# Performance work log

Measured on AMD Instinct MI355X. Metric: run time of the kernel, lower is better.

Reference implementation:

```python
import math
import jax, jax.numpy as jnp
import numpy as np

B, S, G, D = 16, 256, 2048, 512
H = 8
DK = D // H  # per-head key dim
E = 8        # num experts
TOPK = 2


def setup_inputs() -> dict:
    key = jax.random.key(0)
    ks = jax.random.split(key, 12)
    init = lambda k, shape, fan_in: jax.random.uniform(k, shape, jnp.float32, -1.0, 1.0) / np.sqrt(fan_in)
    return {
        'query': jax.random.normal(ks[0], (B, S, D), jnp.float32),
        'key': jax.random.normal(ks[1], (B, G, D), jnp.float32),
        'value': jax.random.normal(ks[2], (B, G, D), jnp.float32),  # unused by module (MHA uses h=key)
        'logit_key': jax.random.normal(ks[3], (B, G, D), jnp.float32),
        'attn_mask': jnp.zeros((B, G), dtype=bool),
        'Wq': init(ks[4], (H, D, DK), D),
        'Wk': init(ks[5], (H, D, DK), D),
        'Wv': init(ks[6], (H, D, DK), D),
        'Wo': init(ks[7], (H, DK, D), DK),
        'w_gate': jnp.zeros((D, E), jnp.float32) + init(ks[8], (D, E), D) * 0.0 + init(ks[9], (D, E), D),
        'expert_w': init(ks[10], (E, D, D), D),
    }


def _mha_glimpse(query, h, attn_mask, Wq, Wk, Wv, Wo):
    # Kool-style MHA: K and V both derived from h
    Q = jnp.einsum('bsd,hdk->bhsk', query, Wq)
    K = jnp.einsum('bgd,hdk->bhgk', h, Wk)
    V = jnp.einsum('bgd,hdk->bhgk', h, Wv)
    scores = jnp.einsum('bhsk,bhgk->bhsg', Q, K) / math.sqrt(DK)
    # 2D mask (B,G) expanded over heads and steps; True = masked out
    mask = attn_mask[:, None, None, :]
    scores = jnp.where(mask, jnp.float32(-1e9), scores)
    attn = jax.nn.softmax(scores, axis=-1)
    heads = jnp.einsum('bhsg,bhgk->bhsk', attn, V)
    return jnp.einsum('bhsk,hkd->bsd', heads, Wo)


def _moe(x, w_gate, expert_w):
    # x: (N, D). Noisy top-k gating, eval mode (no noise): clean logits -> top-k -> softmax over top-k.
    logits = x @ w_gate                                  # (N, E)
    top_vals, top_idx = jax.lax.top_k(logits, TOPK)      # (N, k)
    top_gates = jax.nn.softmax(top_vals, axis=-1)        # (N, k)
    gates = jnp.sum(jax.nn.one_hot(top_idx, E, dtype=x.dtype) * top_gates[..., None], axis=1)  # (N, E)
    expert_out = jnp.einsum('nd,edo->neo', x, expert_w)  # dense combine: same math as dispatch/scatter
    return jnp.einsum('ne,neo->no', gates, expert_out)


def reference(query, key, value, logit_key, attn_mask, Wq, Wk, Wv, Wo, w_gate, expert_w):
    glimpse = _mha_glimpse(query, key, attn_mask, Wq, Wk, Wv, Wo)  # (B, S, D)
    gm = _moe(glimpse.reshape(B * S, D), w_gate, expert_w).reshape(B, S, D)
    logits = jnp.einsum('bsd,bgd->bsg', gm, logit_key) / math.sqrt(D)
    return logits
```

## Files before the change

kernel.cpp:

```cpp
#include <hip/hip_runtime.h>

#define B_  16
#define S_  256
#define G_  2048
#define D_  512
#define H_  8
#define DK_ 64
#define E_  8

typedef _Float16 half8  __attribute__((ext_vector_type(8)));
typedef _Float16 half4v __attribute__((ext_vector_type(4)));
typedef float    floatx4 __attribute__((ext_vector_type(4)));
typedef float    floatx16 __attribute__((ext_vector_type(16)));

#define GLDS(g, l) __builtin_amdgcn_global_load_lds( \
    (const __attribute__((address_space(1))) void*)(g), \
    (__attribute__((address_space(3))) void*)(l), 16, 0, 0)

__global__ void __launch_bounds__(256) split_f16(
    const float* __restrict__ src, _Float16* __restrict__ hi,
    _Float16* __restrict__ lo, int n4)
{
    int i = blockIdx.x * 256 + threadIdx.x;
    if (i >= n4) return;
    float4 v = ((const float4*)src)[i];
    half4v h, l;
    h[0] = (_Float16)v.x; h[1] = (_Float16)v.y;
    h[2] = (_Float16)v.z; h[3] = (_Float16)v.w;
    l[0] = (_Float16)(v.x - (float)h[0]); l[1] = (_Float16)(v.y - (float)h[1]);
    l[2] = (_Float16)(v.z - (float)h[2]); l[3] = (_Float16)(v.w - (float)h[3]);
    ((half4v*)hi)[i] = h;
    ((half4v*)lo)[i] = l;
}

__global__ void __launch_bounds__(256) transpose_split(
    const float* __restrict__ src, _Float16* __restrict__ hi,
    _Float16* __restrict__ lo, int R, int C)
{
    __shared__ float T[32][33];
    const int tid = threadIdx.x;
    const long zo = (long)blockIdx.z * R * C;
    const int r0 = blockIdx.y * 32, c0 = blockIdx.x * 32;
#pragma unroll
    for (int p = 0; p < 4; ++p) {
        int i = tid + p * 256;
        int lr = i >> 5, lc = i & 31;
        T[lr][lc] = src[zo + (long)(r0 + lr) * C + (c0 + lc)];
    }
    __syncthreads();
#pragma unroll
    for (int p = 0; p < 4; ++p) {
        int i = tid + p * 256;
        int orr = i >> 5, oc = i & 31;
        float v = T[oc][orr];
        _Float16 h = (_Float16)v;
        long o = zo + (long)(c0 + orr) * R + (r0 + oc);
        hi[o] = h;
        lo[o] = (_Float16)(v - (float)h);
    }
}

__global__ void __launch_bounds__(512) mask_bitmap(
    const unsigned char* __restrict__ mask, unsigned long long* __restrict__ bmp)
{
    const int t = threadIdx.x;
    const int b = t >> 5, tile = t & 31;
    const unsigned char* m = mask + (long)b * G_ + tile * 64;
    unsigned long long v = 0ULL;
#pragma unroll
    for (int i = 0; i < 64; ++i)
        v |= (unsigned long long)(m[i] ? 1u : 0u) << i;
    bmp[t] = v;
}

__global__ void __launch_bounds__(256) gemm_f16x3(
    const _Float16* __restrict__ Ah, const _Float16* __restrict__ Al,
    const _Float16* __restrict__ Bh, const _Float16* __restrict__ Bl,
    float* __restrict__ C, _Float16* __restrict__ Chi, _Float16* __restrict__ Clo,
    long ldc, long sAz, long sBz, long sCz, float alpha)
{
    __shared__ _Float16 Ash[128 * 32], Asl[128 * 32];
    __shared__ _Float16 Bsh[128 * 32], Bsl[128 * 32];
    const int tid = threadIdx.x;
    const int w = tid >> 6, lane = tid & 63;
    const int quad = lane >> 4, tn = lane & 15;
    const int wm = (w >> 1) * 64, wn = (w & 1) * 64;
    const int z = blockIdx.z;
    const long m0 = (long)blockIdx.y * 128;
    const long n0 = (long)blockIdx.x * 128;
    const _Float16* Agh = Ah + (z * sAz + m0) * 512;
    const _Float16* Agl = Al + (z * sAz + m0) * 512;
    const _Float16* Bgh = Bh + (z * sBz + n0) * 512;
    const _Float16* Bgl = Bl + (z * sBz + n0) * 512;
    const long glane = (long)(lane >> 2) * 512 + (lane & 3) * 8;

    floatx4 acc[4][4] = {};

    for (int k0 = 0; k0 < 512; k0 += 32) {
#pragma unroll
        for (int cc = 0; cc < 2; ++cc) {
            const int c = 2 * w + cc;
            const long go = (long)c * 16 * 512 + glane + k0;
            GLDS(Agh + go, Ash + c * 512);
            GLDS(Agl + go, Asl + c * 512);
            GLDS(Bgh + go, Bsh + c * 512);
            GLDS(Bgl + go, Bsl + c * 512);
        }
        asm volatile("s_waitcnt vmcnt(0)" ::: "memory");
        __syncthreads();

        half8 ah[4], al[4], bh[4], bl[4];
#pragma unroll
        for (int t = 0; t < 4; ++t) {
            ah[t] = *(const half8*)&Ash[(wm + t * 16 + tn) * 32 + quad * 8];
            al[t] = *(const half8*)&Asl[(wm + t * 16 + tn) * 32 + quad * 8];
            bh[t] = *(const half8*)&Bsh[(wn + t * 16 + tn) * 32 + quad * 8];
            bl[t] = *(const half8*)&Bsl[(wn + t * 16 + tn) * 32 + quad * 8];
        }
#pragma unroll
        for (int i = 0; i < 4; ++i)
#pragma unroll
            for (int j = 0; j < 4; ++j) {
                acc[i][j] = __builtin_amdgcn_mfma_f32_16x16x32_f16(ah[i], bh[j], acc[i][j], 0, 0, 0);
                acc[i][j] = __builtin_amdgcn_mfma_f32_16x16x32_f16(ah[i], bl[j], acc[i][j], 0, 0, 0);
                acc[i][j] = __builtin_amdgcn_mfma_f32_16x16x32_f16(al[i], bh[j], acc[i][j], 0, 0, 0);
            }
        __syncthreads();
    }

#pragma unroll
    for (int i = 0; i < 4; ++i) {
        const long row0 = m0 + wm + i * 16 + quad * 4;
#pragma unroll
        for (int r = 0; r < 4; ++r) {
            const long row = row0 + r;
#pragma unroll
            for (int j = 0; j < 4; ++j) {
                float v = acc[i][j][r] * alpha;
                const long o = (long)z * sCz + row * ldc + n0 + wn + j * 16 + tn;
                if (C) C[o] = v;
                if (Chi) {
                    _Float16 hh = (_Float16)v;
                    Chi[o] = hh;
                    Clo[o] = (_Float16)(v - (float)hh);
                }
            }
        }
    }
}

__global__ void __launch_bounds__(256) flash_mfma(
    const _Float16* __restrict__ qh, const _Float16* __restrict__ qlo,
    const _Float16* __restrict__ kh, const _Float16* __restrict__ kl,
    const _Float16* __restrict__ vh, const _Float16* __restrict__ vl,
    const unsigned long long* __restrict__ bmp,
    float* __restrict__ Opart, float* __restrict__ Lpart)
{
    __shared__ half8 KH[512], KL[512], VH[512], VL[512];
    const int tid = threadIdx.x;
    const int wid = tid >> 6, lane = tid & 63;
    const int lh = lane >> 5, ln = lane & 31;
    const int head = blockIdx.y, b = blockIdx.z;
    const int sblk = blockIdx.x & 1, gq = blockIdx.x >> 1;
    const long tok0 = (long)b * S_ + sblk * 128 + wid * 32;

    const long qoff = (tok0 + ln) * 512 + head * 64 + lh * 8;
    half8 qfh[4], qfl[4];
#pragma unroll
    for (int ks = 0; ks < 4; ++ks) {
        qfh[ks] = *(const half8*)(qh + qoff + ks * 16);
        qfl[ks] = *(const half8*)(qlo + qoff + ks * 16);
    }

    const int srow_lo = lane >> 3;
    const int sgs = lane & 7;
    const long kgK = (long)b * G_ * 512 + head * 64;
    const long kgV = (long)head * 64 * (B_ * G_) + (long)b * G_;

    floatx16 accO[2] = {};
    float lsum = 0.f;

    for (int t = 0; t < 8; ++t) {
        const int g0 = gq * 512 + t * 64;
#pragma unroll
        for (int cc = 0; cc < 2; ++cc) {
            const int c = 2 * wid + cc;
            const int r = c * 8 + srow_lo;
            const int gs = sgs ^ (r & 7);
            const long ko = kgK + (long)(g0 + r) * 512 + gs * 8;
            const long vo = kgV + (long)r * (B_ * G_) + g0 + gs * 8;
            GLDS(kh + ko, KH + c * 64);
            GLDS(kl + ko, KL + c * 64);
            GLDS(vh + vo, VH + c * 64);
            GLDS(vl + vo, VL + c * 64);
        }
        asm volatile("s_waitcnt vmcnt(0)" ::: "memory");
        __syncthreads();

        floatx16 accS[2] = {};
#pragma unroll
        for (int gt = 0; gt < 2; ++gt) {
            const int grow = gt * 32 + ln;
            const int gbase = grow * 8, gswz = grow & 7;
#pragma unroll
            for (int ks = 0; ks < 4; ++ks) {
                const int gi = gbase + ((ks * 2 + lh) ^ gswz);
                half8 kbh = KH[gi], kbl = KL[gi];
                accS[gt] = __builtin_amdgcn_mfma_f32_32x32x16_f16(kbh, qfh[ks], accS[gt], 0, 0, 0);
                accS[gt] = __builtin_amdgcn_mfma_f32_32x32x16_f16(kbh, qfl[ks], accS[gt], 0, 0, 0);
                accS[gt] = __builtin_amdgcn_mfma_f32_32x32x16_f16(kbl, qfh[ks], accS[gt], 0, 0, 0);
            }
        }

        const unsigned long long bm = bmp[(b << 5) + (g0 >> 6)];
        if (bm != 0ULL) {
            const unsigned w0 = lh ? ((unsigned)bm >> 4) : (unsigned)bm;
            const unsigned w1 = lh ? ((unsigned)(bm >> 32) >> 4) : (unsigned)(bm >> 32);
#pragma unroll
            for (int gt = 0; gt < 2; ++gt) {
                const unsigned wsel = gt ? w1 : w0;
#pragma unroll
                for (int r = 0; r < 16; ++r) {
                    const int sh = (r & 3) + 8 * (r >> 2);
                    if ((wsel >> sh) & 1u) accS[gt][r] = -1.0e9f;
                }
            }
        }

        float rs = 0.f;
#pragma unroll
        for (int gt = 0; gt < 2; ++gt)
#pragma unroll
            for (int r = 0; r < 16; ++r) {
                const float pv = __builtin_exp2f(accS[gt][r]);
                accS[gt][r] = pv;
                rs += pv;
            }
        rs += __shfl_xor(rs, 32);
        lsum += rs;

#pragma unroll
        for (int gt = 0; gt < 2; ++gt)
#pragma unroll
            for (int w = 0; w < 2; ++w) {
                half8 ph, pl;
#pragma unroll
                for (int j = 0; j < 4; ++j) {
                    const float pA = accS[gt][8 * w + j];
                    const float pB = accS[gt][8 * w + 4 + j];
                    const float snd = lh ? pA : pB;
                    const float rcv = __shfl_xor(snd, 32);
                    const float e03 = lh ? rcv : pA;
                    const float e47 = lh ? pB : rcv;
                    float hi = __uint_as_float(__float_as_uint(e03) & 0xFFFFE000u);
                    ph[j] = (_Float16)hi;
                    pl[j] = (_Float16)(e03 - hi);
                    hi = __uint_as_float(__float_as_uint(e47) & 0xFFFFE000u);
                    ph[4 + j] = (_Float16)hi;
                    pl[4 + j] = (_Float16)(e47 - hi);
                }
                const int gvb = gt * 4 + w * 2 + lh;
#pragma unroll
                for (int nt = 0; nt < 2; ++nt) {
                    const int vrow = nt * 32 + ln;
                    const int gi = vrow * 8 + (gvb ^ (vrow & 7));
                    half8 vbh = VH[gi], vbl = VL[gi];
                    accO[nt] = __builtin_amdgcn_mfma_f32_32x32x16_f16(ph, vbh, accO[nt], 0, 0, 0);
                    accO[nt] = __builtin_amdgcn_mfma_f32_32x32x16_f16(ph, vbl, accO[nt], 0, 0, 0);
                    accO[nt] = __builtin_amdgcn_mfma_f32_32x32x16_f16(pl, vbh, accO[nt], 0, 0, 0);
                }
            }
        __syncthreads();
    }

    float* Op = Opart + (long)gq * (4096L * 512);
#pragma unroll
    for (int nt = 0; nt < 2; ++nt)
#pragma unroll
        for (int r = 0; r < 16; ++r) {
            const int s = (r & 3) + 8 * (r >> 2) + 4 * lh;
            Op[(tok0 + s) * 512 + head * 64 + nt * 32 + ln] = accO[nt][r];
        }
    if (lane < 32)
        Lpart[(long)gq * 32768 + (tok0 + lane) * 8 + head] = lsum;
}

__global__ void __launch_bounds__(256) combine_flash(
    const float* __restrict__ Op, const float* __restrict__ Lp,
    _Float16* __restrict__ hd_hi, _Float16* __restrict__ hd_lo)
{
    const int idx = blockIdx.x * 256 + threadIdx.x;
    const int n = idx >> 7;
    const int c = (idx & 127) * 4;
    const int h = c >> 6;
    float l = 0.f;
#pragma unroll
    for (int q = 0; q < 4; ++q) l += Lp[q * 32768 + (long)n * 8 + h];
    const float inv = 1.0f / l;
    float4 a = *(const float4*)(Op + (long)n * 512 + c);
#pragma unroll
    for (int q = 1; q < 4; ++q) {
        float4 d = *(const float4*)(Op + (long)q * 2097152 + (long)n * 512 + c);
        a.x += d.x; a.y += d.y; a.z += d.z; a.w += d.w;
    }
    const float ox = a.x * inv, oy = a.y * inv, oz = a.z * inv, ow = a.w * inv;
    half4v hh, ll;
    hh[0] = (_Float16)ox; hh[1] = (_Float16)oy;
    hh[2] = (_Float16)oz; hh[3] = (_Float16)ow;
    ll[0] = (_Float16)(ox - (float)hh[0]); ll[1] = (_Float16)(oy - (float)hh[1]);
    ll[2] = (_Float16)(oz - (float)hh[2]); ll[3] = (_Float16)(ow - (float)hh[3]);
    *(half4v*)(hd_hi + (long)n * 512 + c) = hh;
    *(half4v*)(hd_lo + (long)n * 512 + c) = ll;
}

__global__ void __launch_bounds__(256) gate_topk(
    const _Float16* __restrict__ Xh, const _Float16* __restrict__ Xl,
    const float* __restrict__ wg, float* __restrict__ gates)
{
    __shared__ float W[512][8];
    __shared__ float Xs[256][37];
    const int tid = threadIdx.x;
    const int n0 = blockIdx.x * 256;
#pragma unroll
    for (int p = 0; p < 16; ++p) ((float*)W)[tid + p * 256] = wg[tid + p * 256];

    float acc[8] = {};
    for (int dc = 0; dc < 512; dc += 32) {
        __syncthreads();
#pragma unroll
        for (int p = 0; p < 8; ++p) {
            int f = tid + p * 256;
            int row = f >> 3, c4 = f & 7;
            long o = (long)(n0 + row) * 512 + dc + 4 * c4;
            half4v hv = *(const half4v*)(Xh + o);
            half4v lv = *(const half4v*)(Xl + o);
#pragma unroll
            for (int i = 0; i < 4; ++i) Xs[row][4 * c4 + i] = (float)hv[i] + (float)lv[i];
        }
        __syncthreads();
        for (int d2 = 0; d2 < 32; ++d2) {
            float xv = Xs[tid][d2];
#pragma unroll
            for (int e = 0; e < 8; ++e) acc[e] += xv * W[dc + d2][e];
        }
    }
    float v1 = -3.0e38f; int i1 = 0;
#pragma unroll
    for (int e = 0; e < 8; ++e) if (acc[e] > v1) { v1 = acc[e]; i1 = e; }
    float v2 = -3.0e38f; int i2 = -1;
#pragma unroll
    for (int e = 0; e < 8; ++e) if (e != i1 && acc[e] > v2) { v2 = acc[e]; i2 = e; }
    float t = __expf(v2 - v1);
    float g1 = 1.0f / (1.0f + t);
    float g2 = t / (1.0f + t);
#pragma unroll
    for (int e = 0; e < 8; ++e)
        gates[(long)(n0 + tid) * 8 + e] = (e == i1) ? g1 : ((e == i2) ? g2 : 0.0f);
}

__global__ void __launch_bounds__(256) combine_moe(
    const float* __restrict__ eo, const float* __restrict__ gates,
    _Float16* __restrict__ gh, _Float16* __restrict__ gl)
{
    const int idx = blockIdx.x * 256 + threadIdx.x;
    const int n = idx >> 7;
    const int c = (idx & 127) * 4;
    float g[8];
#pragma unroll
    for (int e = 0; e < 8; ++e) g[e] = gates[(long)n * 8 + e];
    float ax = 0.f, ay = 0.f, az = 0.f, aw = 0.f;
#pragma unroll
    for (int e = 0; e < 8; ++e) {
        if (g[e] != 0.0f) {
            float4 v = *(const float4*)(eo + (long)e * 2097152 + (long)n * 512 + c);
            ax += g[e] * v.x; ay += g[e] * v.y; az += g[e] * v.z; aw += g[e] * v.w;
        }
    }
    half4v h, l;
    h[0] = (_Float16)ax; h[1] = (_Float16)ay; h[2] = (_Float16)az; h[3] = (_Float16)aw;
    l[0] = (_Float16)(ax - (float)h[0]); l[1] = (_Float16)(ay - (float)h[1]);
    l[2] = (_Float16)(az - (float)h[2]); l[3] = (_Float16)(aw - (float)h[3]);
    *(half4v*)(gh + (long)n * 512 + c) = h;
    *(half4v*)(gl + (long)n * 512 + c) = l;
}

extern "C" void kernel_launch(void* const* d_in, const int* in_sizes, int n_in,
                              void* d_out, int out_size, void* d_ws, size_t ws_size,
                              hipStream_t stream) {
    const float* query     = (const float*)d_in[0];
    const float* key       = (const float*)d_in[1];
    const float* logit_key = (const float*)d_in[3];
    const unsigned char* mask = (const unsigned char*)d_in[4];
    const float* Wq = (const float*)d_in[5];
    const float* Wk = (const float*)d_in[6];
    const float* Wv = (const float*)d_in[7];
    const float* Wo = (const float*)d_in[8];
    const float* wg = (const float*)d_in[9];
    const float* Ew = (const float*)d_in[10];
    float* out = (float*)d_out;

    const size_t MBy = 1048576;
    char* W = (char*)d_ws;
    _Float16* q_hi  = (_Float16*)(W + 0 * MBy);
    _Float16* q_lo  = (_Float16*)(W + 4 * MBy);
    _Float16* kp_hi = (_Float16*)(W + 8 * MBy);
    _Float16* kp_lo = (_Float16*)(W + 40 * MBy);
    _Float16* vt_hi = (_Float16*)(W + 72 * MBy);
    _Float16* vt_lo = (_Float16*)(W + 104 * MBy);
    _Float16* kin_hi = (_Float16*)(W + 136 * MBy);
    _Float16* kin_lo = (_Float16*)(W + 168 * MBy);
    float*    Opart = (float*)(W + 136 * MBy);
    float*    Lpart = (float*)(W + 168 * MBy);
    float*    eo    = (float*)(W + 136 * MBy);
    _Float16* lk_hi = (_Float16*)(W + 136 * MBy);
    _Float16* lk_lo = (_Float16*)(W + 168 * MBy);
    _Float16* wq_hi = (_Float16*)(W + 204 * MBy);
    _Float16* wq_lo = (_Float16*)(W + 204 * MBy + 524288);
    _Float16* wk_hi = (_Float16*)(W + 205 * MBy);
    _Float16* wk_lo = (_Float16*)(W + 205 * MBy + 524288);
    _Float16* wv_hi = (_Float16*)(W + 206 * MBy);
    _Float16* wv_lo = (_Float16*)(W + 206 * MBy + 524288);
    _Float16* wo_hi = (_Float16*)(W + 207 * MBy);
    _Float16* wo_lo = (_Float16*)(W + 207 * MBy + 524288);
    _Float16* ew_hi = (_Float16*)(W + 208 * MBy);
    _Float16* ew_lo = (_Float16*)(W + 212 * MBy);
    _Float16* qi_hi = (_Float16*)(W + 216 * MBy);
    _Float16* qi_lo = (_Float16*)(W + 220 * MBy);
    _Float16* hd_hi = (_Float16*)(W + 216 * MBy);
    _Float16* hd_lo = (_Float16*)(W + 220 * MBy);
    _Float16* gl_hi = (_Float16*)(W + 224 * MBy);
    _Float16* gl_lo = (_Float16*)(W + 228 * MBy);
    _Float16* gm_hi = (_Float16*)(W + 232 * MBy);
    _Float16* gm_lo = (_Float16*)(W + 236 * MBy);
    float*    gates = (float*)(W + 240 * MBy);
    unsigned long long* bmp = (unsigned long long*)(W + 240 * MBy + 131072);

    dim3 blk(256);

    split_f16<<<dim3(16384), blk, 0, stream>>>(key, kin_hi, kin_lo, 4194304);
    split_f16<<<dim3(2048), blk, 0, stream>>>(query, qi_hi, qi_lo, 524288);
    mask_bitmap<<<dim3(1), dim3(512), 0, stream>>>(mask, bmp);
    transpose_split<<<dim3(2, 16, 8), blk, 0, stream>>>(Wq, wq_hi, wq_lo, 512, 64);
    transpose_split<<<dim3(2, 16, 8), blk, 0, stream>>>(Wk, wk_hi, wk_lo, 512, 64);
    transpose_split<<<dim3(2, 16, 8), blk, 0, stream>>>(Wv, wv_hi, wv_lo, 512, 64);
    transpose_split<<<dim3(16, 16, 1), blk, 0, stream>>>(Wo, wo_hi, wo_lo, 512, 512);
    transpose_split<<<dim3(16, 16, 8), blk, 0, stream>>>(Ew, ew_hi, ew_lo, 512, 512);

    gemm_f16x3<<<dim3(4, 32, 1), blk, 0, stream>>>(
        qi_hi, qi_lo, wq_hi, wq_lo, nullptr, q_hi, q_lo, 512, 0, 0, 0,
        0.1803368801111204f);
    gemm_f16x3<<<dim3(4, 256, 1), blk, 0, stream>>>(
        kin_hi, kin_lo, wk_hi, wk_lo, nullptr, kp_hi, kp_lo, 512, 0, 0, 0, 1.0f);
    gemm_f16x3<<<dim3(256, 4, 1), blk, 0, stream>>>(
        wv_hi, wv_lo, kin_hi, kin_lo, nullptr, vt_hi, vt_lo, (long)B_ * G_,
        0, 0, 0, 1.0f);

    flash_mfma<<<dim3(8, H_, B_), blk, 0, stream>>>(
        q_hi, q_lo, kp_hi, kp_lo, vt_hi, vt_lo, bmp, Opart, Lpart);
    combine_flash<<<dim3(2048), blk, 0, stream>>>(Opart, Lpart, hd_hi, hd_lo);

    gemm_f16x3<<<dim3(4, 32, 1), blk, 0, stream>>>(
        hd_hi, hd_lo, wo_hi, wo_lo, nullptr, gl_hi, gl_lo, 512, 0, 0, 0, 1.0f);

    gate_topk<<<dim3(16), blk, 0, stream>>>(gl_hi, gl_lo, wg, gates);

    gemm_f16x3<<<dim3(4, 32, 8), blk, 0, stream>>>(
        gl_hi, gl_lo, ew_hi, ew_lo, eo, nullptr, nullptr, 512, 0, 512, 2097152, 1.0f);

    combine_moe<<<dim3(2048), blk, 0, stream>>>(eo, gates, gm_hi, gm_lo);

    split_f16<<<dim3(16384), blk, 0, stream>>>(logit_key, lk_hi, lk_lo, 4194304);

    gemm_f16x3<<<dim3(16, 2, 16), blk, 0, stream>>>(
        gm_hi, gm_lo, lk_hi, lk_lo, out, nullptr, nullptr, 2048,
        256, 2048, 524288, 0.04419417382415922f);
}
```

Measured before the change: 617.6 us.

## Replace dense MoE expert GEMM with sparse top-2 token dispatch

Gating now emits top-2 expert indices and gates, and a new kernel builds per-expert token lists with atomics. A gathered GEMM then computes only the routed tokens for each expert, skipping empty tiles, and the combine step reads just the two relevant expert outputs. This removes roughly three quarters of the expert GEMM FLOPs and eo traffic. The cost is an extra launch, atomics, gathered row loads, and load imbalance across experts.

```diff
diff --git a/kernel.cpp b/kernel.cpp
--- a/kernel.cpp
+++ b/kernel.cpp
@@ -61,9 +61,11 @@
 }
 
 __global__ void __launch_bounds__(512) mask_bitmap(
-    const unsigned char* __restrict__ mask, unsigned long long* __restrict__ bmp)
+    const unsigned char* __restrict__ mask, unsigned long long* __restrict__ bmp,
+    int* __restrict__ cnt)
 {
     const int t = threadIdx.x;
+    if (t < 8) cnt[t] = 0;
     const int b = t >> 5, tile = t & 31;
     const unsigned char* m = mask + (long)b * G_ + tile * 64;
     unsigned long long v = 0ULL;
@@ -145,6 +147,83 @@
                     Clo[o] = (_Float16)(v - (float)hh);
                 }
             }
+        }
+    }
+}
+
+__global__ void __launch_bounds__(256) gemm_moe(
+    const _Float16* __restrict__ Ah, const _Float16* __restrict__ Al,
+    const _Float16* __restrict__ Bh, const _Float16* __restrict__ Bl,
+    float* __restrict__ eo, const int* __restrict__ lists,
+    const int* __restrict__ cnt)
+{
+    const int e = blockIdx.z;
+    const int n_e = cnt[e];
+    const int tile = blockIdx.y;
+    if (tile * 128 >= n_e) return;
+
+    __shared__ _Float16 Ash[128 * 32], Asl[128 * 32];
+    __shared__ _Float16 Bsh[128 * 32], Bsl[128 * 32];
+    const int tid = threadIdx.x;
+    const int w = tid >> 6, lane = tid & 63;
+    const int quad = lane >> 4, tn = lane & 15;
+    const int wm = (w >> 1) * 64, wn = (w & 1) * 64;
+    const long n0 = (long)blockIdx.x * 128;
+    const _Float16* Bgh = Bh + ((long)e * 512 + n0) * 512;
+    const _Float16* Bgl = Bl + ((long)e * 512 + n0) * 512;
+    const long glane = (long)(lane >> 2) * 512 + (lane & 3) * 8;
+
+    long arow[2];
+#pragma unroll
+    for (int cc = 0; cc < 2; ++cc) {
+        const int c = 2 * w + cc;
+        const int sl = tile * 128 + c * 16 + (lane >> 2);
+        const int tok = (sl < n_e) ? lists[e * 4096 + sl] : 0;
+        arow[cc] = (long)tok * 512 + (lane & 3) * 8;
+    }
+
+    floatx4 acc[4][4] = {};
+
+    for (int k0 = 0; k0 < 512; k0 += 32) {
+#pragma unroll
+        for (int cc = 0; cc < 2; ++cc) {
+            const int c = 2 * w + cc;
+            const long go = (long)c * 16 * 512 + glane + k0;
+            GLDS(Ah + arow[cc] + k0, Ash + c * 512);
+            GLDS(Al + arow[cc] + k0, Asl + c * 512);
+            GLDS(Bgh + go, Bsh + c * 512);
+            GLDS(Bgl + go, Bsl + c * 512);
+        }
+        asm volatile("s_waitcnt vmcnt(0)" ::: "memory");
+        __syncthreads();
+
+        half8 ah[4], al[4], bh[4], bl[4];
+#pragma unroll
+        for (int t = 0; t < 4; ++t) {
+            ah[t] = *(const half8*)&Ash[(wm + t * 16 + tn) * 32 + quad * 8];
+            al[t] = *(const half8*)&Asl[(wm + t * 16 + tn) * 32 + quad * 8];
+            bh[t] = *(const half8*)&Bsh[(wn + t * 16 + tn) * 32 + quad * 8];
+            bl[t] = *(const half8*)&Bsl[(wn + t * 16 + tn) * 32 + quad * 8];
+        }
+#pragma unroll
+        for (int i = 0; i < 4; ++i)
+#pragma unroll
+            for (int j = 0; j < 4; ++j) {
+                acc[i][j] = __builtin_amdgcn_mfma_f32_16x16x32_f16(ah[i], bh[j], acc[i][j], 0, 0, 0);
+                acc[i][j] = __builtin_amdgcn_mfma_f32_16x16x32_f16(ah[i], bl[j], acc[i][j], 0, 0, 0);
+                acc[i][j] = __builtin_amdgcn_mfma_f32_16x16x32_f16(al[i], bh[j], acc[i][j], 0, 0, 0);
+            }
+        __syncthreads();
+    }
+
+#pragma unroll
+    for (int i = 0; i < 4; ++i) {
+        const long row0 = (long)e * 4096 + tile * 128 + wm + i * 16 + quad * 4;
+#pragma unroll
+        for (int r = 0; r < 4; ++r) {
+#pragma unroll
+            for (int j = 0; j < 4; ++j)
+                eo[(row0 + r) * 512 + n0 + wn + j * 16 + tn] = acc[i][j][r];
         }
     }
 }
@@ -315,7 +394,7 @@
 
 __global__ void __launch_bounds__(256) gate_topk(
     const _Float16* __restrict__ Xh, const _Float16* __restrict__ Xl,
-    const float* __restrict__ wg, float* __restrict__ gates)
+    const float* __restrict__ wg, int* __restrict__ idx2, float2* __restrict__ gv2)
 {
     __shared__ float W[512][8];
     __shared__ float Xs[256][37];
@@ -353,29 +432,46 @@
     float t = __expf(v2 - v1);
     float g1 = 1.0f / (1.0f + t);
     float g2 = t / (1.0f + t);
-#pragma unroll
-    for (int e = 0; e < 8; ++e)
-        gates[(long)(n0 + tid) * 8 + e] = (e == i1) ? g1 : ((e == i2) ? g2 : 0.0f);
+    const int ea = (i1 < i2) ? i1 : i2;
+    const int eb = (i1 < i2) ? i2 : i1;
+    const float ga = (i1 < i2) ? g1 : g2;
+    const float gb = (i1 < i2) ? g2 : g1;
+    idx2[n0 + tid] = ea | (eb << 8);
+    gv2[n0 + tid] = make_float2(ga, gb);
+}
+
+__global__ void __launch_bounds__(256) build_lists(
+    const int* __restrict__ idx2, int* __restrict__ lists,
+    int* __restrict__ cnt, int2* __restrict__ slots2)
+{
+    const int n = blockIdx.x * 256 + threadIdx.x;
+    const int p = idx2[n];
+    const int ea = p & 255, eb = (p >> 8) & 255;
+    const int sa = atomicAdd(&cnt[ea], 1);
+    const int sb = atomicAdd(&cnt[eb], 1);
+    lists[ea * 4096 + sa] = n;
+    lists[eb * 4096 + sb] = n;
+    slots2[n] = make_int2(sa, sb);
 }
 
 __global__ void __launch_bounds__(256) combine_moe(
-    const float* __restrict__ eo, const float* __restrict__ gates,
+    const float* __restrict__ eo, const int* __restrict__ idx2,
+    const float2* __restrict__ gv2, const int2* __restrict__ slots2,
     _Float16* __restrict__ gh, _Float16* __restrict__ gl)
 {
     const int idx = blockIdx.x * 256 + threadIdx.x;
     const int n = idx >> 7;
     const int c = (idx & 127) * 4;
-    float g[8];
-#pragma unroll
-    for (int e = 0; e < 8; ++e) g[e] = gates[(long)n * 8 + e];
-    float ax = 0.f, ay = 0.f, az = 0.f, aw = 0.f;
-#pragma unroll
-    for (int e = 0; e < 8; ++e) {
-        if (g[e] != 0.0f) {
-            float4 v = *(const float4*)(eo + (long)e * 2097152 + (long)n * 512 + c);
-            ax += g[e] * v.x; ay += g[e] * v.y; az += g[e] * v.z; aw += g[e] * v.w;
-        }
-    }
+    const int p = idx2[n];
+    const int2 s = slots2[n];
+    const float2 g = gv2[n];
+    const int ea = p & 255, eb = (p >> 8) & 255;
+    float4 va = *(const float4*)(eo + ((long)ea * 4096 + s.x) * 512 + c);
+    float4 vb = *(const float4*)(eo + ((long)eb * 4096 + s.y) * 512 + c);
+    const float ax = g.x * va.x + g.y * vb.x;
+    const float ay = g.x * va.y + g.y * vb.y;
+    const float az = g.x * va.z + g.y * vb.z;
+    const float aw = g.x * va.w + g.y * vb.w;
     half4v h, l;
     h[0] = (_Float16)ax; h[1] = (_Float16)ay; h[2] = (_Float16)az; h[3] = (_Float16)aw;
     l[0] = (_Float16)(ax - (float)h[0]); l[1] = (_Float16)(ay - (float)h[1]);
@@ -432,14 +528,18 @@
     _Float16* gl_lo = (_Float16*)(W + 228 * MBy);
     _Float16* gm_hi = (_Float16*)(W + 232 * MBy);
     _Float16* gm_lo = (_Float16*)(W + 236 * MBy);
-    float*    gates = (float*)(W + 240 * MBy);
+    float2*   gv2   = (float2*)(W + 240 * MBy);
+    int2*     slots2= (int2*)(W + 240 * MBy + 32768);
+    int*      idx2  = (int*)(W + 240 * MBy + 65536);
     unsigned long long* bmp = (unsigned long long*)(W + 240 * MBy + 131072);
+    int*      lists = (int*)(W + 240 * MBy + 135168);
+    int*      cnt   = (int*)(W + 240 * MBy + 266240);
 
     dim3 blk(256);
 
     split_f16<<<dim3(16384), blk, 0, stream>>>(key, kin_hi, kin_lo, 4194304);
     split_f16<<<dim3(2048), blk, 0, stream>>>(query, qi_hi, qi_lo, 524288);
-    mask_bitmap<<<dim3(1), dim3(512), 0, stream>>>(mask, bmp);
+    mask_bitmap<<<dim3(1), dim3(512), 0, stream>>>(mask, bmp, cnt);
     transpose_split<<<dim3(2, 16, 8), blk, 0, stream>>>(Wq, wq_hi, wq_lo, 512, 64);
     transpose_split<<<dim3(2, 16, 8), blk, 0, stream>>>(Wk, wk_hi, wk_lo, 512, 64);
     transpose_split<<<dim3(2, 16, 8), blk, 0, stream>>>(Wv, wv_hi, wv_lo, 512, 64);
@@ -462,12 +562,13 @@
     gemm_f16x3<<<dim3(4, 32, 1), blk, 0, stream>>>(
         hd_hi, hd_lo, wo_hi, wo_lo, nullptr, gl_hi, gl_lo, 512, 0, 0, 0, 1.0f);
 
-    gate_topk<<<dim3(16), blk, 0, stream>>>(gl_hi, gl_lo, wg, gates);
-
-    gemm_f16x3<<<dim3(4, 32, 8), blk, 0, stream>>>(
-        gl_hi, gl_lo, ew_hi, ew_lo, eo, nullptr, nullptr, 512, 0, 512, 2097152, 1.0f);
-
-    combine_moe<<<dim3(2048), blk, 0, stream>>>(eo, gates, gm_hi, gm_lo);
+    gate_topk<<<dim3(16), blk, 0, stream>>>(gl_hi, gl_lo, wg, idx2, gv2);
+    build_lists<<<dim3(16), blk, 0, stream>>>(idx2, lists, cnt, slots2);
+
+    gemm_moe<<<dim3(4, 32, 8), blk, 0, stream>>>(
+        gl_hi, gl_lo, ew_hi, ew_lo, eo, lists, cnt);
+
+    combine_moe<<<dim3(2048), blk, 0, stream>>>(eo, idx2, gv2, slots2, gm_hi, gm_lo);
 
     split_f16<<<dim3(16384), blk, 0, stream>>>(logit_key, lk_hi, lk_lo, 4194304);
 
```

Measured after the change: 664.7 us. 1.08x slower.
